# Performance work log

Measured on AMD Instinct MI355X. Metric: run time of the kernel, lower is better.

## Reference

```python
import jax, jax.numpy as jnp
import numpy as np

NUM_EXPERTS = 64
TOP_K = 2


def setup_inputs() -> dict:
    key = jax.random.key(0)
    k1, k2 = jax.random.split(key)
    # [batch, seq_len, d_model] token activations
    x = jax.random.normal(k1, (4, 4096, 2048), dtype=jnp.float32)
    # router_dense weight (no bias): [d_model, num_experts]
    W = jax.random.normal(k2, (2048, NUM_EXPERTS), dtype=jnp.float32) * 0.02
    return {"x": x, "W": W}


def reference(x, W):
    # router logits: [B, S, E]
    router_logits = jnp.einsum("bsd,de->bse", x, W)
    # softmax router (router_type == 'softmax')
    router_probs = jax.nn.softmax(router_logits, axis=-1)
    # top-k expert selection per token (sorted=False in TF; value set identical)
    top_k_probs, top_k_indices = jax.lax.top_k(router_probs, TOP_K)
    # dispatch tensor: sum of one-hots == tensor_scatter_nd_add of ones -> [B, S, E]
    dispatch_tensor = jax.nn.one_hot(top_k_indices, NUM_EXPERTS, dtype=router_probs.dtype).sum(axis=-2)
    return dispatch_tensor, router_probs, top_k_probs, top_k_indices
```

## Files before the change

kernel.cpp:

```cpp
#include <hip/hip_runtime.h>

#define TTOT 16384
#define DDIM 2048
#define NEXP 64
#define TPB  32
#define KCH  256
#define W3TERM (NEXP * DDIM)

typedef __attribute__((ext_vector_type(8))) short bf16x8;
typedef __attribute__((ext_vector_type(4))) float f32x4;
typedef __attribute__((ext_vector_type(4))) unsigned int u32x4;

__device__ __forceinline__ void split3(const f32x4 va, const f32x4 vb,
                                       bf16x8& h, bf16x8& m, bf16x8& l)
{
    const float f[8] = {va.x, va.y, va.z, va.w, vb.x, vb.y, vb.z, vb.w};
    unsigned int hu[8], mu[8], lu[8];
#pragma unroll
    for (int j = 0; j < 8; ++j) {
        const unsigned int xb = __float_as_uint(f[j]);
        const unsigned int hb = xb & 0xffff0000u;
        const float r1 = f[j] - __uint_as_float(hb);
        const unsigned int mb = __float_as_uint(r1) & 0xffff0000u;
        const float r2 = r1 - __uint_as_float(mb);
        hu[j] = hb; mu[j] = mb; lu[j] = __float_as_uint(r2);
    }
    u32x4 hw, mw, lw;
#pragma unroll
    for (int w = 0; w < 4; ++w) {
        hw[w] = (hu[2 * w] >> 16) | (mu[2 * w] & 0u) | (hu[2 * w + 1] & 0xffff0000u);
        mw[w] = (mu[2 * w] >> 16) | (mu[2 * w + 1] & 0xffff0000u);
        lw[w] = (lu[2 * w] >> 16) | (lu[2 * w + 1] & 0xffff0000u);
    }
    h = __builtin_bit_cast(bf16x8, hw);
    m = __builtin_bit_cast(bf16x8, mw);
    l = __builtin_bit_cast(bf16x8, lw);
}

__global__ __launch_bounds__(256)
void w_split(const float* __restrict__ W, unsigned short* __restrict__ W3)
{
    const int q = blockIdx.x * 256 + threadIdx.x;
    const int e = q >> 11;
    const int d = q & 2047;
    const float w = W[(size_t)d * NEXP + e];
    const unsigned int xb = __float_as_uint(w);
    const unsigned int hb = xb & 0xffff0000u;
    const float r1 = w - __uint_as_float(hb);
    const unsigned int mb = __float_as_uint(r1) & 0xffff0000u;
    const float r2 = r1 - __uint_as_float(mb);
    const unsigned int lb = __float_as_uint(r2);
    const size_t o = (size_t)e * DDIM + d;
    W3[o]              = (unsigned short)(hb >> 16);
    W3[o + W3TERM]     = (unsigned short)(mb >> 16);
    W3[o + 2 * W3TERM] = (unsigned short)(lb >> 16);
}

__global__ __launch_bounds__(512, 2)
void moe_gemm(const float* __restrict__ x, const unsigned short* __restrict__ W3,
              float* __restrict__ out)
{
    __shared__ float L[TPB][NEXP + 1];
    const int tid  = threadIdx.x;
    const int lane = tid & 63;
    const int wq   = __builtin_amdgcn_readfirstlane(tid >> 6);
    const int lrow = lane & 15;
    const int lk   = lane >> 4;
    const int tokBase = blockIdx.x * TPB;

    f32x4 c[2][4];
#pragma unroll
    for (int mt = 0; mt < 2; ++mt)
#pragma unroll
        for (int nt = 0; nt < 4; ++nt)
            c[mt][nt] = (f32x4){0.0f, 0.0f, 0.0f, 0.0f};

    const int kBase = wq * KCH;
    const float* xp0 = x + (size_t)(tokBase + lrow) * DDIM + kBase + lk * 8;
    const float* xp1 = xp0 + (size_t)16 * DDIM;
    const unsigned short* wp = W3 + (size_t)lrow * DDIM + kBase + lk * 8;

    f32x4 r0a = *(const f32x4*)(xp0);
    f32x4 r0b = *(const f32x4*)(xp0 + 4);
    f32x4 r1a = *(const f32x4*)(xp1);
    f32x4 r1b = *(const f32x4*)(xp1 + 4);

    for (int ks = 0; ks < KCH / 32; ++ks) {
        const f32x4 c0a = r0a, c0b = r0b, c1a = r1a, c1b = r1b;
        if (ks < KCH / 32 - 1) {
            const float* nx0 = xp0 + (ks + 1) * 32;
            const float* nx1 = xp1 + (ks + 1) * 32;
            r0a = *(const f32x4*)(nx0);
            r0b = *(const f32x4*)(nx0 + 4);
            r1a = *(const f32x4*)(nx1);
            r1b = *(const f32x4*)(nx1 + 4);
        }

        bf16x8 bh[4], bm[4], bl[4];
#pragma unroll
        for (int nt = 0; nt < 4; ++nt) {
            const unsigned short* bp = wp + (size_t)nt * 16 * DDIM + ks * 32;
            bh[nt] = *(const bf16x8*)(bp);
            bm[nt] = *(const bf16x8*)(bp + W3TERM);
            bl[nt] = *(const bf16x8*)(bp + 2 * W3TERM);
        }

        bf16x8 ah0, am0, al0, ah1, am1, al1;
        split3(c0a, c0b, ah0, am0, al0);
        split3(c1a, c1b, ah1, am1, al1);

#pragma unroll
        for (int nt = 0; nt < 4; ++nt) c[0][nt] = __builtin_amdgcn_mfma_f32_16x16x32_bf16(ah0, bh[nt], c[0][nt], 0, 0, 0);
#pragma unroll
        for (int nt = 0; nt < 4; ++nt) c[1][nt] = __builtin_amdgcn_mfma_f32_16x16x32_bf16(ah1, bh[nt], c[1][nt], 0, 0, 0);
#pragma unroll
        for (int nt = 0; nt < 4; ++nt) c[0][nt] = __builtin_amdgcn_mfma_f32_16x16x32_bf16(ah0, bm[nt], c[0][nt], 0, 0, 0);
#pragma unroll
        for (int nt = 0; nt < 4; ++nt) c[1][nt] = __builtin_amdgcn_mfma_f32_16x16x32_bf16(ah1, bm[nt], c[1][nt], 0, 0, 0);
#pragma unroll
        for (int nt = 0; nt < 4; ++nt) c[0][nt] = __builtin_amdgcn_mfma_f32_16x16x32_bf16(am0, bh[nt], c[0][nt], 0, 0, 0);
#pragma unroll
        for (int nt = 0; nt < 4; ++nt) c[1][nt] = __builtin_amdgcn_mfma_f32_16x16x32_bf16(am1, bh[nt], c[1][nt], 0, 0, 0);
#pragma unroll
        for (int nt = 0; nt < 4; ++nt) c[0][nt] = __builtin_amdgcn_mfma_f32_16x16x32_bf16(ah0, bl[nt], c[0][nt], 0, 0, 0);
#pragma unroll
        for (int nt = 0; nt < 4; ++nt) c[1][nt] = __builtin_amdgcn_mfma_f32_16x16x32_bf16(ah1, bl[nt], c[1][nt], 0, 0, 0);
#pragma unroll
        for (int nt = 0; nt < 4; ++nt) c[0][nt] = __builtin_amdgcn_mfma_f32_16x16x32_bf16(al0, bh[nt], c[0][nt], 0, 0, 0);
#pragma unroll
        for (int nt = 0; nt < 4; ++nt) c[1][nt] = __builtin_amdgcn_mfma_f32_16x16x32_bf16(al1, bh[nt], c[1][nt], 0, 0, 0);
#pragma unroll
        for (int nt = 0; nt < 4; ++nt) c[0][nt] = __builtin_amdgcn_mfma_f32_16x16x32_bf16(am0, bm[nt], c[0][nt], 0, 0, 0);
#pragma unroll
        for (int nt = 0; nt < 4; ++nt) c[1][nt] = __builtin_amdgcn_mfma_f32_16x16x32_bf16(am1, bm[nt], c[1][nt], 0, 0, 0);
    }

    for (int w = 0; w < 8; ++w) {
        if (wq == w) {
#pragma unroll
            for (int mt = 0; mt < 2; ++mt)
#pragma unroll
                for (int nt = 0; nt < 4; ++nt)
#pragma unroll
                    for (int i = 0; i < 4; ++i) {
                        const int row = mt * 16 + lk * 4 + i;
                        const int col = nt * 16 + lrow;
                        if (w == 0) L[row][col]  = c[mt][nt][i];
                        else        L[row][col] += c[mt][nt][i];
                    }
        }
        __syncthreads();
    }

    float* dispatch = out;
    float* probs    = out + (size_t)TTOT * NEXP;
    float* tkp      = out + (size_t)2 * TTOT * NEXP;
    float* tki      = tkp + (size_t)TTOT * 2;

#pragma unroll
    for (int tt = 0; tt < 4; ++tt) {
        const int te = wq * 4 + tt;
        const int gt = tokBase + te;
        const float Lg = L[te][lane];

        float m = Lg;
#pragma unroll
        for (int off = 32; off; off >>= 1) m = fmaxf(m, __shfl_xor(m, off, 64));
        const float p = expf(Lg - m);
        float sden = p;
#pragma unroll
        for (int off = 32; off; off >>= 1) sden += __shfl_xor(sden, off, 64);
        const float prob = p / sden;

        float v1 = prob; int i1 = lane;
#pragma unroll
        for (int off = 32; off; off >>= 1) {
            const float ov = __shfl_xor(v1, off, 64);
            const int   oi = __shfl_xor(i1, off, 64);
            if (ov > v1 || (ov == v1 && oi < i1)) { v1 = ov; i1 = oi; }
        }
        float v2 = (lane == i1) ? -1.0f : prob; int i2 = lane;
#pragma unroll
        for (int off = 32; off; off >>= 1) {
            const float ov = __shfl_xor(v2, off, 64);
            const int   oi = __shfl_xor(i2, off, 64);
            if (ov > v2 || (ov == v2 && oi < i2)) { v2 = ov; i2 = oi; }
        }

        probs[(size_t)gt * NEXP + lane]    = prob;
        dispatch[(size_t)gt * NEXP + lane] = (lane == i1 || lane == i2) ? 1.0f : 0.0f;
        if (lane == 0) {
            tkp[(size_t)gt * 2 + 0] = v1;
            tkp[(size_t)gt * 2 + 1] = v2;
            tki[(size_t)gt * 2 + 0] = (float)i1;
            tki[(size_t)gt * 2 + 1] = (float)i2;
        }
    }
}

extern "C" void kernel_launch(void* const* d_in, const int* in_sizes, int n_in,
                              void* d_out, int out_size, void* d_ws, size_t ws_size,
                              hipStream_t stream) {
    const float* x = (const float*)d_in[0];
    const float* W = (const float*)d_in[1];
    float* out = (float*)d_out;
    unsigned short* W3 = (unsigned short*)d_ws;

    w_split<<<512, 256, 0, stream>>>(W, W3);
    moe_gemm<<<TTOT / TPB, 512, 0, stream>>>(x, W3, out);
}
```

Before: 239.8 us.

## Stage x through swizzled LDS with async global_load_lds and repack W layout

Activations are no longer loaded straight into registers. Each wave now streams its 32-token by 32-column x slice into double-buffered shared memory using global_load_lds, with an XOR swizzle to avoid bank conflicts, and reads the fragments back from LDS. The split W is repacked into an interleaved [d/8][expert][8] layout so each lane's B fragment loads are contiguous, and launch bounds are raised to 4 blocks per CU. The aim is better coalesced x loads and more memory-level parallelism on this bandwidth-bound GEMV-like GEMM. In exchange it adds 64KB+ of LDS per block, which may limit the occupancy that launch_bounds requests, and it relies on a vmcnt(0) wait for synchronization.

```diff
diff --git a/kernel.cpp b/kernel.cpp
--- a/kernel.cpp
+++ b/kernel.cpp
@@ -5,7 +5,8 @@
 #define NEXP 64
 #define TPB  32
 #define KCH  256
-#define W3TERM (NEXP * DDIM)
+#define NKS  8
+#define WTERM (NEXP * DDIM)
 
 typedef __attribute__((ext_vector_type(8))) short bf16x8;
 typedef __attribute__((ext_vector_type(4))) float f32x4;
@@ -28,7 +29,7 @@
     u32x4 hw, mw, lw;
 #pragma unroll
     for (int w = 0; w < 4; ++w) {
-        hw[w] = (hu[2 * w] >> 16) | (mu[2 * w] & 0u) | (hu[2 * w + 1] & 0xffff0000u);
+        hw[w] = (hu[2 * w] >> 16) | (hu[2 * w + 1] & 0xffff0000u);
         mw[w] = (mu[2 * w] >> 16) | (mu[2 * w + 1] & 0xffff0000u);
         lw[w] = (lu[2 * w] >> 16) | (lu[2 * w + 1] & 0xffff0000u);
     }
@@ -38,7 +39,7 @@
 }
 
 __global__ __launch_bounds__(256)
-void w_split(const float* __restrict__ W, unsigned short* __restrict__ W3)
+void w_split(const float* __restrict__ W, unsigned short* __restrict__ W4)
 {
     const int q = blockIdx.x * 256 + threadIdx.x;
     const int e = q >> 11;
@@ -50,16 +51,17 @@
     const unsigned int mb = __float_as_uint(r1) & 0xffff0000u;
     const float r2 = r1 - __uint_as_float(mb);
     const unsigned int lb = __float_as_uint(r2);
-    const size_t o = (size_t)e * DDIM + d;
-    W3[o]              = (unsigned short)(hb >> 16);
-    W3[o + W3TERM]     = (unsigned short)(mb >> 16);
-    W3[o + 2 * W3TERM] = (unsigned short)(lb >> 16);
-}
-
-__global__ __launch_bounds__(512, 2)
-void moe_gemm(const float* __restrict__ x, const unsigned short* __restrict__ W3,
+    const size_t o = ((size_t)(d >> 3) * 64 + e) * 8 + (d & 7);
+    W4[o]             = (unsigned short)(hb >> 16);
+    W4[o + WTERM]     = (unsigned short)(mb >> 16);
+    W4[o + 2 * WTERM] = (unsigned short)(lb >> 16);
+}
+
+__global__ __launch_bounds__(512, 4)
+void moe_gemm(const float* __restrict__ x, const unsigned short* __restrict__ W4,
               float* __restrict__ out)
 {
+    __shared__ float xs[2][8][32][32];
     __shared__ float L[TPB][NEXP + 1];
     const int tid  = threadIdx.x;
     const int lane = tid & 63;
@@ -67,6 +69,7 @@
     const int lrow = lane & 15;
     const int lk   = lane >> 4;
     const int tokBase = blockIdx.x * TPB;
+    const int kBase   = wq * KCH;
 
     f32x4 c[2][4];
 #pragma unroll
@@ -75,36 +78,54 @@
         for (int nt = 0; nt < 4; ++nt)
             c[mt][nt] = (f32x4){0.0f, 0.0f, 0.0f, 0.0f};
 
-    const int kBase = wq * KCH;
-    const float* xp0 = x + (size_t)(tokBase + lrow) * DDIM + kBase + lk * 8;
-    const float* xp1 = xp0 + (size_t)16 * DDIM;
-    const unsigned short* wp = W3 + (size_t)lrow * DDIM + kBase + lk * 8;
-
-    f32x4 r0a = *(const f32x4*)(xp0);
-    f32x4 r0b = *(const f32x4*)(xp0 + 4);
-    f32x4 r1a = *(const f32x4*)(xp1);
-    f32x4 r1b = *(const f32x4*)(xp1 + 4);
-
-    for (int ks = 0; ks < KCH / 32; ++ks) {
-        const f32x4 c0a = r0a, c0b = r0b, c1a = r1a, c1b = r1b;
-        if (ks < KCH / 32 - 1) {
-            const float* nx0 = xp0 + (ks + 1) * 32;
-            const float* nx1 = xp1 + (ks + 1) * 32;
-            r0a = *(const f32x4*)(nx0);
-            r0b = *(const f32x4*)(nx0 + 4);
-            r1a = *(const f32x4*)(nx1);
-            r1b = *(const f32x4*)(nx1 + 4);
-        }
+    const int srow = lane >> 3;
+    const int scol = (lane & 7) ^ srow;
+    const float* sBase = x + (size_t)(tokBase + srow) * DDIM + kBase + scol * 4;
+
+#define STAGE(ksn, dstbuf)                                                     \
+    {                                                                          \
+        const float* g_ = sBase + (ksn) * 32;                                  \
+        float* l_ = &xs[dstbuf][wq][0][0];                                     \
+        _Pragma("unroll")                                                      \
+        for (int cc = 0; cc < 4; ++cc)                                         \
+            __builtin_amdgcn_global_load_lds(                                  \
+                (const __attribute__((address_space(1))) unsigned int*)        \
+                    (g_ + cc * 8 * DDIM),                                      \
+                (__attribute__((address_space(3))) unsigned int*)              \
+                    (l_ + cc * 256),                                           \
+                16, 0, 0);                                                     \
+    }
+
+    const int ph    = (lk * 2) ^ (lrow & 7);
+    const int aoff0 = lrow * 32 + ph * 4;
+    const int aoff1 = (16 + lrow) * 32 + ph * 4;
+
+    const unsigned short* bph = W4 + (size_t)(((kBase >> 3) + lk) * 512 + lrow * 8);
+    const unsigned short* bpm = bph + WTERM;
+    const unsigned short* bpl = bpm + WTERM;
+
+    STAGE(0, 0)
+
+#pragma unroll 2
+    for (int ks = 0; ks < NKS; ++ks) {
+        asm volatile("s_waitcnt vmcnt(0)" ::: "memory");
+        const int buf = ks & 1;
+        if (ks + 1 < NKS) STAGE(ks + 1, buf ^ 1)
 
         bf16x8 bh[4], bm[4], bl[4];
 #pragma unroll
         for (int nt = 0; nt < 4; ++nt) {
-            const unsigned short* bp = wp + (size_t)nt * 16 * DDIM + ks * 32;
-            bh[nt] = *(const bf16x8*)(bp);
-            bm[nt] = *(const bf16x8*)(bp + W3TERM);
-            bl[nt] = *(const bf16x8*)(bp + 2 * W3TERM);
-        }
-
+            bh[nt] = *(const bf16x8*)(bph + nt * 128);
+            bm[nt] = *(const bf16x8*)(bpm + nt * 128);
+            bl[nt] = *(const bf16x8*)(bpl + nt * 128);
+        }
+        bph += 2048; bpm += 2048; bpl += 2048;
+
+        const float* sub = &xs[buf][wq][0][0];
+        const f32x4 c0a = *(const f32x4*)(sub + aoff0);
+        const f32x4 c0b = *(const f32x4*)(sub + (aoff0 ^ 4));
+        const f32x4 c1a = *(const f32x4*)(sub + aoff1);
+        const f32x4 c1b = *(const f32x4*)(sub + (aoff1 ^ 4));
         bf16x8 ah0, am0, al0, ah1, am1, al1;
         split3(c0a, c0b, ah0, am0, al0);
         split3(c1a, c1b, ah1, am1, al1);
@@ -134,6 +155,7 @@
 #pragma unroll
         for (int nt = 0; nt < 4; ++nt) c[1][nt] = __builtin_amdgcn_mfma_f32_16x16x32_bf16(am1, bm[nt], c[1][nt], 0, 0, 0);
     }
+#undef STAGE
 
     for (int w = 0; w < 8; ++w) {
         if (wq == w) {
@@ -204,8 +226,8 @@
     const float* x = (const float*)d_in[0];
     const float* W = (const float*)d_in[1];
     float* out = (float*)d_out;
-    unsigned short* W3 = (unsigned short*)d_ws;
-
-    w_split<<<512, 256, 0, stream>>>(W, W3);
-    moe_gemm<<<TTOT / TPB, 512, 0, stream>>>(x, W3, out);
-}
+    unsigned short* W4 = (unsigned short*)d_ws;
+
+    w_split<<<512, 256, 0, stream>>>(W, W4);
+    moe_gemm<<<TTOT / TPB, 512, 0, stream>>>(x, W4, out);
+}
```

Measured after the change: 215.1 us. 10.3% less time.
